# Kernel tuning notes

Hardware: AMD Instinct MI355X
Metric: run time of the kernel (lower is better)

Reference implementation:

```python
import jax, jax.numpy as jnp
import numpy as np

N_HEAD = 16


def _rotate_half(x):
    # interleaved split then concat, exactly as the torch module does
    x1 = x[..., ::2]
    x2 = x[..., 1::2]
    return jnp.concatenate((-x2, x1), axis=-1)


def setup_inputs() -> dict:
    key = jax.random.key(0)
    k1, k2, k3 = jax.random.split(key, 3)
    B, T, C = 4, 2048, 2048
    x = jax.random.normal(k1, (B, T, C), dtype=jnp.float32)
    w_attn = jax.random.normal(k2, (3 * C, C), dtype=jnp.float32) * 0.02
    b_attn = jnp.zeros((3 * C,), dtype=jnp.float32)
    w_proj = jax.random.normal(k3, (C, C), dtype=jnp.float32) * 0.02
    b_proj = jnp.zeros((C,), dtype=jnp.float32)
    return {"x": x, "w_attn": w_attn, "b_attn": b_attn, "w_proj": w_proj, "b_proj": b_proj}


def reference(x, w_attn, b_attn, w_proj, b_proj):
    B, T, C = x.shape
    H = N_HEAD
    D = C // H

    qkv = x @ w_attn.T + b_attn  # (B, T, 3C)
    q, k, v = jnp.split(qkv, 3, axis=2)
    # (B, H, T, D)
    q = q.reshape(B, T, H, D).transpose(0, 2, 1, 3)
    k = k.reshape(B, T, H, D).transpose(0, 2, 1, 3)
    v = v.reshape(B, T, H, D).transpose(0, 2, 1, 3)

    # RoPE tables (buffer inv_freq computed from head_dim)
    inv_freq = 1.0 / (10000.0 ** (jnp.arange(0, D, 2, dtype=jnp.float32) / D))
    t = jnp.arange(T, dtype=jnp.float32)
    freqs = t[:, None] * inv_freq[None, :]            # (T, D/2)
    emb = jnp.concatenate((freqs, freqs), axis=-1)    # (T, D)
    cos, sin = jnp.cos(emb), jnp.sin(emb)

    # module's (nonstandard) rotary application: returns q_cos + q_sin
    rq, rk = _rotate_half(q), _rotate_half(k)
    q = (q * cos - rq * sin) + (q * sin + rq * cos)
    k = (k * cos - rk * sin) + (k * sin + rk * cos)

    # causal SDPA
    scale = 1.0 / jnp.sqrt(jnp.asarray(D, dtype=x.dtype))
    scores = jnp.einsum("bhqd,bhkd->bhqk", q, k) * scale
    causal = jnp.tril(jnp.ones((T, T), dtype=bool))
    scores = jnp.where(causal, scores, jnp.asarray(-1e30, dtype=scores.dtype))
    att = jax.nn.softmax(scores, axis=-1)
    y = jnp.einsum("bhqk,bhkd->bhqd", att, v)

    y = y.transpose(0, 2, 1, 3).reshape(B, T, C)
    return y @ w_proj.T + b_proj
```

## Files before the change

kernel.cpp:

```cpp
#include <hip/hip_runtime.h>

#define T_SEQ 2048
#define DHEAD 128
#define NHEAD 16
#define CDIM  2048
#define BATCH 4

typedef __bf16 v8bf __attribute__((ext_vector_type(8)));
typedef __bf16 v4bf __attribute__((ext_vector_type(4)));
typedef __bf16 v2bf __attribute__((ext_vector_type(2)));
typedef float  v4f  __attribute__((ext_vector_type(4)));

#define MFMA16(a,b,c) __builtin_amdgcn_mfma_f32_16x16x32_bf16(a,b,c,0,0,0)
#define GLDS16(g,l) __builtin_amdgcn_global_load_lds( \
    (__attribute__((address_space(1))) void*)(g), \
    (__attribute__((address_space(3))) void*)(l), 16, 0, 0)

__global__ __launch_bounds__(256) void cvt_all(const float* __restrict__ x,
                                               const float* __restrict__ wa,
                                               const float* __restrict__ wp,
                                               __bf16* __restrict__ xo,
                                               __bf16* __restrict__ wao,
                                               __bf16* __restrict__ wpo,
                                               float2* __restrict__ rt) {
  int i = blockIdx.x * 256 + threadIdx.x;
  int stride = gridDim.x * 256;
  for (int j = i; j < 8519680; j += stride) {
    if (j < 8388608) {
      const float* src; __bf16* dst; int off;
      if (j < 4194304)      { src = x;  dst = xo;  off = j; }
      else if (j < 7340032) { src = wa; dst = wao; off = j - 4194304; }
      else                  { src = wp; dst = wpo; off = j - 7340032; }
      float4 v = *(const float4*)(src + (size_t)off * 4);
      v4bf o = {(__bf16)v.x, (__bf16)v.y, (__bf16)v.z, (__bf16)v.w};
      *(v4bf*)(dst + (size_t)off * 4) = o;
    } else {
      int e = j - 8388608;
      int tt = e >> 6, jj = e & 63;
      float invf = exp2f((float)jj * (-13.287712379549449f / 64.f));
      float ang = (float)tt * invf;
      float c = cosf(ang), s = sinf(ang);
      rt[e] = make_float2(c + s, c - s);
    }
  }
}

#define LGKM0() { asm volatile("s_waitcnt lgkmcnt(0)" ::: "memory"); \
                  __builtin_amdgcn_sched_barrier(0); }
#define BARR()  { __builtin_amdgcn_s_barrier(); __builtin_amdgcn_sched_barrier(0); }

#define RDA(mm, kk) (*(const v8bf*)(bA + (wm16 + (mm)*32 + lr) * 128 + ((((kk)*64) + lgc) ^ swl)))
#define RDB(n, kk)  (*(const v8bf*)(bB + (wn64 + (n)*16 + lr) * 128 + ((((kk)*64) + lgc) ^ swl)))
#define MF(mm,n,kk) acc[mm][n] = MFMA16(af[(mm)&1][kk], bfr[n][kk], acc[mm][n]);

#define PH_MFMA(MM0, MM1) \
  BARR(); LGKM0(); \
  __builtin_amdgcn_s_setprio(1); \
  MF(MM0,0,0) MF(MM0,1,0) MF(MM0,2,0) MF(MM0,3,0) \
  MF(MM1,0,0) MF(MM1,1,0) MF(MM1,2,0) MF(MM1,3,0) \
  MF(MM0,0,1) MF(MM0,1,1) MF(MM0,2,1) MF(MM0,3,1) \
  MF(MM1,0,1) MF(MM1,1,1) MF(MM1,2,1) MF(MM1,3,1) \
  __builtin_amdgcn_s_setprio(0); \
  BARR();

#define STAGE_H(SRC, ks, hh, LBASE) { \
  GLDS16((SRC) + (size_t)((hh)*128)      * 2048 + (size_t)(ks)*64, lds + (LBASE) + dst0); \
  GLDS16((SRC) + (size_t)((hh)*128 + 64) * 2048 + (size_t)(ks)*64, lds + (LBASE) + 4096 + dst0); }

#define TILE(CB, ks1, ks2) { \
  const char* bA = (const char*)(lds + (CB)*32768); \
  const char* bB = bA + 32768; \
  v8bf bfr[4][2], af[2][2]; \
  af[0][0]=RDA(0,0); af[0][1]=RDA(0,1); af[1][0]=RDA(1,0); af[1][1]=RDA(1,1); \
  bfr[0][0]=RDB(0,0); bfr[0][1]=RDB(0,1); bfr[1][0]=RDB(1,0); bfr[1][1]=RDB(1,1); \
  bfr[2][0]=RDB(2,0); bfr[2][1]=RDB(2,1); bfr[3][0]=RDB(3,0); bfr[3][1]=RDB(3,1); \
  STAGE_H(Asrc, ks1, 1, ((CB)^1)*32768 + 8192); \
  PH_MFMA(0, 1) \
  af[0][0]=RDA(2,0); af[0][1]=RDA(2,1); af[1][0]=RDA(3,0); af[1][1]=RDA(3,1); \
  STAGE_H(Bsrc, ks2, 0, (CB)*32768 + 16384); \
  PH_MFMA(2, 3) \
  af[0][0]=RDA(4,0); af[0][1]=RDA(4,1); af[1][0]=RDA(5,0); af[1][1]=RDA(5,1); \
  STAGE_H(Asrc, ks2, 0, (CB)*32768); \
  PH_MFMA(4, 5) \
  af[0][0]=RDA(6,0); af[0][1]=RDA(6,1); af[1][0]=RDA(7,0); af[1][1]=RDA(7,1); \
  STAGE_H(Bsrc, ks2, 1, (CB)*32768 + 24576); \
  asm volatile("s_waitcnt vmcnt(6)" ::: "memory"); \
  PH_MFMA(6, 7) \
}

__device__ __forceinline__ void gemm256_core(
    const __bf16* __restrict__ A, const __bf16* __restrict__ Bm,
    int row0, int col0, __bf16* lds, v4f (&acc)[8][4],
    int wm16, int wn64, int lr, int lg) {
  int t = threadIdx.x;
  int wid = t >> 6;
  int lgc = lg * 16;
  int swl = (lr & 7) << 4;
#pragma unroll
  for (int mm = 0; mm < 8; ++mm)
#pragma unroll
    for (int n = 0; n < 4; ++n) acc[mm][n] = (v4f){0.f, 0.f, 0.f, 0.f};

  int srow = t >> 3;
  int scol = (((t & 7) ^ ((t >> 3) & 7)) << 3);
  const __bf16* Asrc = A  + (size_t)(row0 + srow) * 2048 + scol;
  const __bf16* Bsrc = Bm + (size_t)(col0 + srow) * 2048 + scol;
  int dst0 = wid << 9;

  STAGE_H(Asrc, 0, 0, 0);
  STAGE_H(Asrc, 0, 1, 8192);
  STAGE_H(Bsrc, 0, 0, 16384);
  STAGE_H(Bsrc, 0, 1, 24576);
  STAGE_H(Bsrc, 1, 0, 32768 + 16384);
  STAGE_H(Asrc, 1, 0, 32768);
  STAGE_H(Bsrc, 1, 1, 32768 + 24576);
  asm volatile("s_waitcnt vmcnt(6)" ::: "memory");
  BARR();

  for (int m = 0; m < 32; m += 2) {
    TILE(0, m + 1, (m + 2) & 31)
    TILE(1, (m + 2) & 31, (m + 3) & 31)
  }
  asm volatile("s_waitcnt vmcnt(0)" ::: "memory");
}

__global__ __launch_bounds__(512, 2) void gemm_qkv8(
    const __bf16* __restrict__ A, const __bf16* __restrict__ Bm,
    const float* __restrict__ bias, const float2* __restrict__ rt,
    __bf16* __restrict__ Qb, __bf16* __restrict__ Kb, __bf16* __restrict__ Vt) {
  extern __shared__ __bf16 lds[];
  int t = threadIdx.x, wid = t >> 6, l = t & 63;
  int lr = l & 15, lg = l >> 4;
  int wm16 = (wid >> 2) * 16, wn64 = (wid & 3) * 64;
  int bid = blockIdx.x;
  int xcd = bid & 7, idx = bid >> 3;
  int row0 = (xcd * 4 + idx / 24) * 256;
  int col0 = (idx % 24) * 256;
  v4f acc[8][4];
  gemm256_core(A, Bm, row0, col0, lds, acc, wm16, wn64, lr, lg);

  if (col0 >= 4096) {
    int h0 = (col0 & 2047) >> 7;
    int bb = row0 >> 11;
    int t0 = row0 & 2047;
    int d_r = t >> 1, half = t & 1;
    int hh = h0 + (d_r >> 7), dd = d_r & 127;
#pragma unroll
    for (int mm = 0; mm < 8; ++mm) {
      __syncthreads();
#pragma unroll
      for (int n = 0; n < 4; ++n) {
        int d_loc = wn64 + n * 16 + lr;
        float bv = bias[col0 + d_loc];
        v4bf pv = {(__bf16)(acc[mm][n][0] + bv), (__bf16)(acc[mm][n][1] + bv),
                   (__bf16)(acc[mm][n][2] + bv), (__bf16)(acc[mm][n][3] + bv)};
        *(v4bf*)&lds[d_loc * 40 + wm16 + lg * 4] = pv;
      }
      __syncthreads();
      size_t vbase = ((size_t)((bb * NHEAD + hh) * DHEAD + dd)) * T_SEQ
                   + t0 + mm * 32 + half * 16;
      v8bf x0 = *(const v8bf*)&lds[d_r * 40 + half * 16];
      v8bf x1 = *(const v8bf*)&lds[d_r * 40 + half * 16 + 8];
      *(v8bf*)&Vt[vbase] = x0;
      *(v8bf*)&Vt[vbase + 8] = x1;
    }
    return;
  }

  __syncthreads();
#pragma unroll
  for (int n = 0; n < 4; ++n) {
    int c_loc = wn64 + n * 16 + lr;
    float bv = bias[col0 + c_loc];
#pragma unroll
    for (int mm = 0; mm < 8; ++mm) {
#pragma unroll
      for (int rr = 0; rr < 4; ++rr) {
        int r_loc = wm16 + mm * 32 + lg * 4 + rr;
        *(__bf16*)((char*)lds + r_loc * 512 + ((2 * c_loc) ^ ((r_loc & 31) << 4)))
            = (__bf16)(acc[mm][n][rr] + bv);
      }
    }
  }
  __syncthreads();
  {
    int tensor = col0 >> 11;
    int h0 = (col0 & 2047) >> 7;
    int bb = row0 >> 11;
    int t0 = row0 & 2047;
    __bf16* QK = tensor ? Kb : Qb;
    int d = l;
    float sgn = (d < 32) ? -1.f : 1.f;
    int mOff = 4 * d;
    int pOff = (d < 32) ? (8 * d) : (8 * d - 256);
    int tOff = ((2 * d) & 63) * 8;
#pragma unroll 4
    for (int i = 0; i < 64; ++i) {
      int p = wid * 64 + i;
      int u = p >> 8, r = p & 255;
      int tt = t0 + r;
      const char* lrow_ = (const char*)lds + r * 512;
      int swz = (r & 31) << 4;
      int cb = u * 256;
      v2bf xm = *(const v2bf*)(lrow_ + ((cb + mOff) ^ swz));
      v4bf xp = *(const v4bf*)(lrow_ + ((cb + pOff) ^ swz));
      float4 tv = *(const float4*)((const char*)(rt + (size_t)tt * 64) + tOff);
      float p1 = (d < 32) ? (float)xp[1] : (float)xp[0];
      float p2 = (d < 32) ? (float)xp[3] : (float)xp[2];
      float o1 = (float)xm[0] * tv.x + sgn * p1 * tv.y;
      float o2 = (float)xm[1] * tv.z + sgn * p2 * tv.w;
      v2bf ov = {(__bf16)o1, (__bf16)o2};
      __bf16* dst = QK + ((size_t)(bb * NHEAD + h0 + u) * T_SEQ + tt) * DHEAD;
      *(v2bf*)(dst + 2 * d) = ov;
    }
  }
}

__global__ __launch_bounds__(512, 2) void gemm_out8(
    const __bf16* __restrict__ A, const __bf16* __restrict__ Bm,
    const float* __restrict__ bias, float* __restrict__ C) {
  extern __shared__ __bf16 lds[];
  int t = threadIdx.x, wid = t >> 6, l = t & 63;
  int lr = l & 15, lg = l >> 4;
  int wm16 = (wid >> 2) * 16, wn64 = (wid & 3) * 64;
  int bid = blockIdx.x;
  int xcd = bid & 7, idx = bid >> 3;
  int row0 = (xcd * 4 + idx / 8) * 256;
  int col0 = (idx % 8) * 256;
  v4f acc[8][4];
  gemm256_core(A, Bm, row0, col0, lds, acc, wm16, wn64, lr, lg);
#pragma unroll
  for (int n = 0; n < 4; ++n) {
    int col = col0 + wn64 + n * 16 + lr;
    float bv = bias[col];
#pragma unroll
    for (int mm = 0; mm < 8; ++mm) {
#pragma unroll
      for (int rr = 0; rr < 4; ++rr) {
        int mg = row0 + wm16 + mm * 32 + lg * 4 + rr;
        C[(size_t)mg * CDIM + col] = acc[mm][n][rr] + bv;
      }
    }
  }
}

__global__ __launch_bounds__(512, 2) void attn_fwd(
    const __bf16* __restrict__ Qb, const __bf16* __restrict__ Kb,
    const __bf16* __restrict__ Vt, __bf16* __restrict__ Y) {
  __shared__ __bf16 lK[64 * 128];
  __shared__ __bf16 lV[128 * 64];
  __shared__ __bf16 plds[8][32][72];
  int t = threadIdx.x, w = t >> 6, l = t & 63;
  int lr = l & 15, lg = l >> 4;
  int id = blockIdx.x;
  int xcd = id & 7, s = id >> 3;
  int bh = xcd * 8 + (s & 7);
  int g = s >> 3;
  int k = (g < 4) ? (7 - g) : (g - 4);
  int qb = k * 256;
  int b = bh >> 4, h = bh & 15;
  int q0 = qb + w * 32;
  const __bf16* Qh = Qb + (size_t)bh * T_SEQ * DHEAD;
  const __bf16* Kh = Kb + (size_t)bh * T_SEQ * DHEAD;
  const __bf16* Vh = Vt + (size_t)bh * DHEAD * T_SEQ;

  v8bf qf[2][4];
#pragma unroll
  for (int j = 0; j < 2; ++j)
#pragma unroll
    for (int c = 0; c < 4; ++c)
      qf[j][c] = *(const v8bf*)&Qh[(size_t)(q0 + j * 16 + lr) * DHEAD + c * 32 + lg * 8];

  v4f o[2][8];
#pragma unroll
  for (int j = 0; j < 2; ++j)
#pragma unroll
    for (int c = 0; c < 8; ++c) o[j][c] = (v4f){0.f, 0.f, 0.f, 0.f};
  float mrow[2] = {-1e30f, -1e30f}, lrow[2] = {0.f, 0.f};
  const float SCALE2 = 0.12751743f;

  int kRow = t >> 4;
  int kSrc = (((t & 15) * 16) ^ ((kRow & 7) << 4)) >> 1;
  int vRow = t >> 3;
  int vSrc = (((t & 7) * 16) ^ ((vRow & 7) << 4)) >> 1;
  __bf16* lKd0 = lK + w * 512 + l * 8;
  __bf16* lKd1 = lK + 4096 + w * 512 + l * 8;
  __bf16* lVd0 = lV + w * 512 + l * 8;
  __bf16* lVd1 = lV + 4096 + w * 512 + l * 8;

  v8bf kr0 = *(const v8bf*)&Kh[(size_t)(kRow) * DHEAD + kSrc];
  v8bf kr1 = *(const v8bf*)&Kh[(size_t)(32 + kRow) * DHEAD + kSrc];
  v8bf vr0 = *(const v8bf*)&Vh[(size_t)(vRow) * T_SEQ + vSrc];
  v8bf vr1 = *(const v8bf*)&Vh[(size_t)(64 + vRow) * T_SEQ + vSrc];

  int kvEnd = qb + 192;
  for (int kv0 = 0; kv0 <= kvEnd; kv0 += 64) {
    __syncthreads();
    *(v8bf*)lKd0 = kr0; *(v8bf*)lKd1 = kr1;
    *(v8bf*)lVd0 = vr0; *(v8bf*)lVd1 = vr1;
    __syncthreads();
    if (kv0 + 64 <= kvEnd) {
      kr0 = *(const v8bf*)&Kh[(size_t)(kv0 + 64 + kRow) * DHEAD + kSrc];
      kr1 = *(const v8bf*)&Kh[(size_t)(kv0 + 96 + kRow) * DHEAD + kSrc];
      vr0 = *(const v8bf*)&Vh[(size_t)(vRow) * T_SEQ + kv0 + 64 + vSrc];
      vr1 = *(const v8bf*)&Vh[(size_t)(64 + vRow) * T_SEQ + kv0 + 64 + vSrc];
    }

    if (kv0 <= q0 + 31) {
      v4f s2[2][4];
#pragma unroll
      for (int j = 0; j < 2; ++j)
#pragma unroll
        for (int f = 0; f < 4; ++f) s2[j][f] = (v4f){0.f, 0.f, 0.f, 0.f};
#pragma unroll
      for (int f = 0; f < 4; ++f) {
        int row = f * 16 + lr;
        int sw = (row & 7) << 4;
#pragma unroll
        for (int c = 0; c < 4; ++c) {
          v8bf kf = *(const v8bf*)((const char*)lK + row * 256 + ((c * 64 + lg * 16) ^ sw));
          s2[0][f] = MFMA16(kf, qf[0][c], s2[0][f]);
          s2[1][f] = MFMA16(kf, qf[1][c], s2[1][f]);
        }
      }

      v8bf pa[2][2];
#pragma unroll
      for (int j = 0; j < 2; ++j) {
        int qg = q0 + j * 16 + lr;
        bool needMask = (kv0 + 63 > q0 + j * 16);
        float p[16];
        float mt = -1e30f;
#pragma unroll
        for (int f = 0; f < 4; ++f)
#pragma unroll
          for (int r = 0; r < 4; ++r) {
            float v = s2[j][f][r] * SCALE2;
            if (needMask && (kv0 + f * 16 + lg * 4 + r > qg)) v = -1e30f;
            p[f * 4 + r] = v;
            mt = fmaxf(mt, v);
          }
        mt = fmaxf(mt, __shfl_xor(mt, 16));
        mt = fmaxf(mt, __shfl_xor(mt, 32));
        if (!__all(mt <= mrow[j] + 8.0f)) {
          float mnew = fmaxf(mrow[j], mt);
          float corr = exp2f(mrow[j] - mnew);
          mrow[j] = mnew;
          lrow[j] *= corr;
          float cf[4];
#pragma unroll
          for (int r = 0; r < 4; ++r) cf[r] = __shfl(corr, lg * 4 + r);
#pragma unroll
          for (int c = 0; c < 8; ++c)
#pragma unroll
            for (int r = 0; r < 4; ++r) o[j][c][r] *= cf[r];
        }
        float psum = 0.f;
#pragma unroll
        for (int r = 0; r < 16; ++r) { p[r] = exp2f(p[r] - mrow[j]); psum += p[r]; }
        psum += __shfl_xor(psum, 16);
        psum += __shfl_xor(psum, 32);
        lrow[j] += psum;
#pragma unroll
        for (int f = 0; f < 4; ++f) {
          v4bf pv = {(__bf16)p[f * 4], (__bf16)p[f * 4 + 1],
                     (__bf16)p[f * 4 + 2], (__bf16)p[f * 4 + 3]};
          *(v4bf*)&plds[w][j * 16 + lr][f * 16 + lg * 4] = pv;
        }
        asm volatile("s_waitcnt lgkmcnt(0)" ::: "memory");
        pa[j][0] = *(const v8bf*)&plds[w][j * 16 + lr][lg * 8];
        pa[j][1] = *(const v8bf*)&plds[w][j * 16 + lr][32 + lg * 8];
      }

#pragma unroll
      for (int c = 0; c < 8; ++c) {
        int row = c * 16 + lr;
        int sw = (row & 7) << 4;
        v8bf vf0 = *(const v8bf*)((const char*)lV + row * 128 + ((lg * 16) ^ sw));
        v8bf vf1 = *(const v8bf*)((const char*)lV + row * 128 + ((64 + lg * 16) ^ sw));
        o[0][c] = MFMA16(pa[0][0], vf0, o[0][c]);
        o[0][c] = MFMA16(pa[0][1], vf1, o[0][c]);
        o[1][c] = MFMA16(pa[1][0], vf0, o[1][c]);
        o[1][c] = MFMA16(pa[1][1], vf1, o[1][c]);
      }
    }
  }

  size_t ybase = ((size_t)b * T_SEQ) * CDIM + (size_t)h * DHEAD;
#pragma unroll
  for (int j = 0; j < 2; ++j) {
    float lf[4];
#pragma unroll
    for (int r = 0; r < 4; ++r) lf[r] = __shfl(lrow[j], lg * 4 + r);
#pragma unroll
    for (int c = 0; c < 8; ++c) {
#pragma unroll
      for (int r = 0; r < 4; ++r) {
        int qq = q0 + j * 16 + lg * 4 + r;
        Y[ybase + (size_t)qq * CDIM + c * 16 + lr] = (__bf16)(o[j][c][r] / lf[r]);
      }
    }
  }
}

extern "C" void kernel_launch(void* const* d_in, const int* in_sizes, int n_in,
                              void* d_out, int out_size, void* d_ws, size_t ws_size,
                              hipStream_t stream) {
  const float* x      = (const float*)d_in[0];
  const float* w_attn = (const float*)d_in[1];
  const float* b_attn = (const float*)d_in[2];
  const float* w_proj = (const float*)d_in[3];
  const float* b_proj = (const float*)d_in[4];
  float* out = (float*)d_out;

  char* ws = (char*)d_ws;
  __bf16* xbf  = (__bf16*)(ws);
  __bf16* wabf = (__bf16*)(ws + 33554432);
  __bf16* wpbf = (__bf16*)(ws + 58720256);
  __bf16* Qb   = (__bf16*)(ws + 67108864);
  __bf16* Kb   = (__bf16*)(ws + 100663296);
  __bf16* Vt   = (__bf16*)(ws + 134217728);
  float2* rtab = (float2*)(ws + 167772160);
  __bf16* Y    = xbf;

  (void)hipFuncSetAttribute((const void*)gemm_qkv8,
                            hipFuncAttributeMaxDynamicSharedMemorySize, 131072);
  (void)hipFuncSetAttribute((const void*)gemm_out8,
                            hipFuncAttributeMaxDynamicSharedMemorySize, 131072);

  cvt_all<<<2048, 256, 0, stream>>>(x, w_attn, w_proj, xbf, wabf, wpbf, rtab);

  gemm_qkv8<<<768, 512, 131072, stream>>>(xbf, wabf, b_attn, rtab, Qb, Kb, Vt);

  attn_fwd<<<512, 512, 0, stream>>>(Qb, Kb, Vt, Y);

  gemm_out8<<<256, 512, 131072, stream>>>(Y, wpbf, b_proj, out);
}
```

Before: 428.1 us.

## Vectorize RoPE epilogue to 16-byte stores and raise wave priority around MFMA blocks

```diff
diff --git a/kernel.cpp b/kernel.cpp
--- a/kernel.cpp
+++ b/kernel.cpp
@@ -189,29 +189,46 @@
     int bb = row0 >> 11;
     int t0 = row0 & 2047;
     __bf16* QK = tensor ? Kb : Qb;
-    int d = l;
-    float sgn = (d < 32) ? -1.f : 1.f;
-    int mOff = 4 * d;
-    int pOff = (d < 32) ? (8 * d) : (8 * d - 256);
-    int tOff = ((2 * d) & 63) * 8;
-#pragma unroll 4
-    for (int i = 0; i < 64; ++i) {
-      int p = wid * 64 + i;
-      int u = p >> 8, r = p & 255;
+#pragma unroll 2
+    for (int i = 0; i < 16; ++i) {
+      int gidx = i * 512 + t;
+      int dh = gidx & 15;
+      int u  = (gidx >> 4) & 1;
+      int r  = gidx >> 5;
       int tt = t0 + r;
       const char* lrow_ = (const char*)lds + r * 512;
       int swz = (r & 31) << 4;
-      int cb = u * 256;
-      v2bf xm = *(const v2bf*)(lrow_ + ((cb + mOff) ^ swz));
-      v4bf xp = *(const v4bf*)(lrow_ + ((cb + pOff) ^ swz));
-      float4 tv = *(const float4*)((const char*)(rt + (size_t)tt * 64) + tOff);
-      float p1 = (d < 32) ? (float)xp[1] : (float)xp[0];
-      float p2 = (d < 32) ? (float)xp[3] : (float)xp[2];
-      float o1 = (float)xm[0] * tv.x + sgn * p1 * tv.y;
-      float o2 = (float)xm[1] * tv.z + sgn * p2 * tv.w;
-      v2bf ov = {(__bf16)o1, (__bf16)o2};
-      __bf16* dst = QK + ((size_t)(bb * NHEAD + h0 + u) * T_SEQ + tt) * DHEAD;
-      *(v2bf*)(dst + 2 * d) = ov;
+      int cb  = u * 256;
+      bool lo = dh < 8;
+      float sgn = lo ? -1.f : 1.f;
+      v8bf xm  = *(const v8bf*)(lrow_ + ((cb + 16 * dh) ^ swz));
+      int pb = cb + 32 * dh - (lo ? 0 : 256);
+      v8bf xp0 = *(const v8bf*)(lrow_ + (pb ^ swz));
+      v8bf xp1 = *(const v8bf*)(lrow_ + ((pb + 16) ^ swz));
+      const float2* tb = rt + (size_t)tt * 64 + ((8 * dh) & 63);
+      float4 t0v = *(const float4*)(tb);
+      float4 t1v = *(const float4*)(tb + 2);
+      float4 t2v = *(const float4*)(tb + 4);
+      float4 t3v = *(const float4*)(tb + 6);
+      float p0 = lo ? (float)xp0[1] : (float)xp0[0];
+      float p1 = lo ? (float)xp0[3] : (float)xp0[2];
+      float p2 = lo ? (float)xp0[5] : (float)xp0[4];
+      float p3 = lo ? (float)xp0[7] : (float)xp0[6];
+      float p4 = lo ? (float)xp1[1] : (float)xp1[0];
+      float p5 = lo ? (float)xp1[3] : (float)xp1[2];
+      float p6 = lo ? (float)xp1[5] : (float)xp1[4];
+      float p7 = lo ? (float)xp1[7] : (float)xp1[6];
+      v8bf ov;
+      ov[0] = (__bf16)((float)xm[0] * t0v.x + sgn * p0 * t0v.y);
+      ov[1] = (__bf16)((float)xm[1] * t0v.z + sgn * p1 * t0v.w);
+      ov[2] = (__bf16)((float)xm[2] * t1v.x + sgn * p2 * t1v.y);
+      ov[3] = (__bf16)((float)xm[3] * t1v.z + sgn * p3 * t1v.w);
+      ov[4] = (__bf16)((float)xm[4] * t2v.x + sgn * p4 * t2v.y);
+      ov[5] = (__bf16)((float)xm[5] * t2v.z + sgn * p5 * t2v.w);
+      ov[6] = (__bf16)((float)xm[6] * t3v.x + sgn * p6 * t3v.y);
+      ov[7] = (__bf16)((float)xm[7] * t3v.z + sgn * p7 * t3v.w);
+      __bf16* dst = QK + ((size_t)(bb * NHEAD + h0 + u) * T_SEQ + tt) * DHEAD + 8 * dh;
+      *(v8bf*)dst = ov;
     }
   }
 }
@@ -312,6 +329,7 @@
       for (int j = 0; j < 2; ++j)
 #pragma unroll
         for (int f = 0; f < 4; ++f) s2[j][f] = (v4f){0.f, 0.f, 0.f, 0.f};
+      __builtin_amdgcn_s_setprio(1);
 #pragma unroll
       for (int f = 0; f < 4; ++f) {
         int row = f * 16 + lr;
@@ -323,6 +341,7 @@
           s2[1][f] = MFMA16(kf, qf[1][c], s2[1][f]);
         }
       }
+      __builtin_amdgcn_s_setprio(0);
 
       v8bf pa[2][2];
 #pragma unroll
@@ -372,6 +391,7 @@
         pa[j][1] = *(const v8bf*)&plds[w][j * 16 + lr][32 + lg * 8];
       }
 
+      __builtin_amdgcn_s_setprio(1);
 #pragma unroll
       for (int c = 0; c < 8; ++c) {
         int row = c * 16 + lr;
@@ -383,6 +403,7 @@
         o[1][c] = MFMA16(pa[1][0], vf0, o[1][c]);
         o[1][c] = MFMA16(pa[1][1], vf1, o[1][c]);
       }
+      __builtin_amdgcn_s_setprio(0);
     }
   }
 
```

Result: slower. 436.8 us (+2.0%).
